# Performance work log

Hardware: AMD Instinct MI355X
Metric: run time of the kernel (lower is better)

The kernel has to match this reference:

```python
import jax, jax.numpy as jnp
import numpy as np

B = 4096
P_HID = 1024
H_HID = 512
MAX_P = 128
MAX_HE = MAX_P // 3  # 42
TAU = 1.0
EPS = 1e-20


def setup_inputs() -> dict:
    key = jax.random.key(0)
    ks = jax.random.split(key, 12)
    s_p = 1.0 / np.sqrt(P_HID)
    s_h = 1.0 / np.sqrt(H_HID)
    # gumbel noise: g = -log(-log(U))
    u_p = jax.random.uniform(ks[3], (B, MAX_P, 2), minval=EPS, maxval=1.0)
    u_h = jax.random.uniform(ks[4], (B, MAX_HE, 2), minval=EPS, maxval=1.0)
    return {
        "particle_h": jax.random.normal(ks[0], (B, P_HID), jnp.float32),
        "edge_h": jax.random.normal(ks[1], (B, H_HID), jnp.float32),
        "hyperedge_h": jax.random.normal(ks[2], (B, H_HID), jnp.float32),
        "g_p": -jnp.log(-jnp.log(u_p)),
        "g_h": -jnp.log(-jnp.log(u_h)),
        "W1_p": jax.random.normal(ks[5], (P_HID, P_HID), jnp.float32) * s_p,
        "b1_p": jnp.zeros((P_HID,), jnp.float32),
        "W2_p": jax.random.normal(ks[6], (P_HID, MAX_P), jnp.float32) * s_p,
        "b2_p": jnp.zeros((MAX_P,), jnp.float32),
        "W1_h": jax.random.normal(ks[7], (H_HID, H_HID), jnp.float32) * s_h,
        "b1_h": jnp.zeros((H_HID,), jnp.float32),
        "W2_h": jax.random.normal(ks[8], (H_HID, MAX_HE), jnp.float32) * s_h,
        "b2_h": jnp.zeros((MAX_HE,), jnp.float32),
    }


def _gumbel_hard_st(logits, g, tau):
    """F.gumbel_softmax(stack([l,-l],-1), tau, hard=True)[...,0] (straight-through)."""
    y = jax.nn.softmax((jnp.stack([logits, -logits], axis=-1) + g) / tau, axis=-1)
    y0 = y[..., 0]
    hard0 = (y0 > y[..., 1]).astype(y0.dtype)
    return hard0 + y0 - jax.lax.stop_gradient(y0)


def _mlp(x, W1, b1, W2, b2):
    return jax.nn.gelu(x @ W1 + b1, approximate=False) @ W2 + b2


def reference(particle_h, edge_h, hyperedge_h, g_p, g_h,
              W1_p, b1_p, W2_p, b2_p, W1_h, b1_h, W2_h, b2_h):
    particle_logits = _mlp(particle_h, W1_p, b1_p, W2_p, b2_p)      # [B, MAX_P]
    particle_mask = _gumbel_hard_st(particle_logits, g_p, TAU)      # [B, MAX_P]
    n_particles = particle_mask.sum(axis=-1).astype(jnp.int32)      # [B]

    # Ragged edge lists as a fixed padded buffer: all C(MAX_P,2) lexicographic
    # pairs (same order as torch.combinations); pair (i,j), i<j, is valid for
    # batch b iff j < n_particles[b].
    ii, jj = jnp.triu_indices(MAX_P, k=1)
    edge_index = jnp.stack([ii, jj]).astype(jnp.int32)              # [2, E_max]
    edge_valid = jj[None, :] < n_particles[:, None]                 # [B, E_max] bool

    hyperedge_logits = _mlp(hyperedge_h, W1_h, b1_h, W2_h, b2_h)    # [B, MAX_HE]
    hyperedge_mask = _gumbel_hard_st(hyperedge_logits, g_h, TAU)
    n_hyperedges = hyperedge_mask.sum(axis=-1).astype(jnp.int32)

    return (particle_mask, n_particles, edge_index, edge_valid,
            hyperedge_mask, n_hyperedges)
```

## Files before the change

kernel.cpp:

```cpp
#include <hip/hip_runtime.h>
#include <hip/hip_bf16.h>
#include <math.h>

typedef __bf16 bf16_t;
typedef bf16_t bf16x8 __attribute__((ext_vector_type(8)));
typedef bf16_t bf16x4 __attribute__((ext_vector_type(4)));
typedef float f32x4 __attribute__((ext_vector_type(4)));
typedef int i32x4 __attribute__((ext_vector_type(4)));
typedef unsigned int u32;

#define B_SZ 4096
#define P_HID 1024
#define H_HID 512
#define MAX_P 128
#define MAX_HE 42
#define HE_PAD 128
#define E_MAX 8128
#define E_MAX4 2032

__device__ __forceinline__ void async_cp16(const bf16_t* g, bf16_t* l) {
    __builtin_amdgcn_global_load_lds(
        (const __attribute__((address_space(1))) u32*)g,
        (__attribute__((address_space(3))) u32*)l, 16, 0, 0);
}

__device__ __forceinline__ float gelu_exact(float v) {
    return 0.5f * v * (1.f + erff(v * 0.70710678118654752f));
}

struct GemmP {
    const bf16_t *Ahi, *Alo, *BThi, *BTlo;
    const float* bias;
    bf16_t *Chi, *Clo;
    const float* g;
    float *out_mask, *out_n;
    int *ws_n;
    int N, K, NV, nx;
};

template<int MODE, int BM>
__global__ __launch_bounds__(256, 3) void gemm_pack(GemmP P, GemmP H, int pBlocks)
{
    constexpr int BN = 128;
    constexpr int MT = BM / 16;
    constexpr int NT = 4;
    constexpr int OPS_A = BM / 16;
    constexpr int OPS_B = BN / 16;
    constexpr int NOPS = 2 * OPS_A + 2 * OPS_B;
    constexpr int TILE = NOPS * 16 * 32;

    __shared__ __align__(16) bf16_t smem[2 * TILE];
    __shared__ float cnt[BM][2];

    const bool isP = (int)blockIdx.x < pBlocks;
    const GemmP& a = isP ? P : H;
    const int bid  = isP ? blockIdx.x : blockIdx.x - pBlocks;
    const int bn   = (bid % a.nx) * BN;
    const int bm   = (bid / a.nx) * BM;
    const int K    = a.K;

    const int tid  = threadIdx.x;
    const int lane = tid & 63;
    const int wid  = tid >> 6;
    const int wn   = wid & 1;
    const int pair = wid >> 1;

    const int srow = lane >> 2;
    const int scol = (lane & 3) * 8;
    const int fr   = lane & 15;
    const int fq   = lane >> 4;

    f32x4 acc[MT][NT];
#pragma unroll
    for (int i = 0; i < MT; ++i)
#pragma unroll
        for (int j = 0; j < NT; ++j)
            acc[i][j] = (f32x4){0.f, 0.f, 0.f, 0.f};

    const bf16_t* const gA0 = a.Ahi  + (size_t)bm * K;
    const bf16_t* const gA1 = a.Alo  + (size_t)bm * K;
    const bf16_t* const gB0 = a.BThi + (size_t)bn * K;
    const bf16_t* const gB1 = a.BTlo + (size_t)bn * K;

    bf16_t* const Tme = smem + pair * TILE;

    for (int kt = 0; kt < K; kt += 64) {
        __syncthreads();
#pragma unroll
        for (int o = 0; o < 2 * NOPS; ++o) {
            if ((o & 3) != wid) continue;
            const int half = (o < NOPS) ? 0 : 1;
            const int oo   = o - half * NOPS;
            const bf16_t* gsrc;
            int q, sec;
            if (oo < OPS_A)                  { q = oo;                     gsrc = gA0; sec = 0; }
            else if (oo < 2 * OPS_A)         { q = oo - OPS_A;             gsrc = gA1; sec = BM * 32; }
            else if (oo < 2 * OPS_A + OPS_B) { q = oo - 2 * OPS_A;         gsrc = gB0; sec = 2 * BM * 32; }
            else                             { q = oo - 2 * OPS_A - OPS_B; gsrc = gB1; sec = 2 * BM * 32 + BN * 32; }
            async_cp16(gsrc + (size_t)(q * 16 + srow) * K + kt + half * 32 + scol,
                       smem + half * TILE + sec + q * 16 * 32);
        }
        __syncthreads();

        bf16x8 ah[MT], al[MT];
#pragma unroll
        for (int i = 0; i < MT; ++i) {
            const int row = i * 16 + fr;
            ah[i] = *(const bf16x8*)(Tme + row * 32 + fq * 8);
            al[i] = *(const bf16x8*)(Tme + BM * 32 + row * 32 + fq * 8);
        }
#pragma unroll
        for (int j = 0; j < NT; ++j) {
            const int row = wn * 64 + j * 16 + fr;
            const bf16x8 bh = *(const bf16x8*)(Tme + 2 * BM * 32 + row * 32 + fq * 8);
            const bf16x8 bl = *(const bf16x8*)(Tme + 2 * BM * 32 + BN * 32 + row * 32 + fq * 8);
#pragma unroll
            for (int i = 0; i < MT; ++i) {
                acc[i][j] = __builtin_amdgcn_mfma_f32_16x16x32_bf16(ah[i], bh, acc[i][j], 0, 0, 0);
                acc[i][j] = __builtin_amdgcn_mfma_f32_16x16x32_bf16(ah[i], bl, acc[i][j], 0, 0, 0);
                acc[i][j] = __builtin_amdgcn_mfma_f32_16x16x32_bf16(al[i], bh, acc[i][j], 0, 0, 0);
            }
        }
    }

    float* const cb = (float*)smem;
    __syncthreads();
    if (pair == 1) {
#pragma unroll
        for (int i = 0; i < MT; ++i)
#pragma unroll
            for (int j = 0; j < NT; ++j)
#pragma unroll
                for (int r = 0; r < 4; ++r)
                    cb[(i * 16 + fq * 4 + r) * BN + wn * 64 + j * 16 + fr] = acc[i][j][r];
    }
    __syncthreads();

    if (pair == 0) {
#pragma unroll
        for (int i = 0; i < MT; ++i)
#pragma unroll
            for (int j = 0; j < NT; ++j)
#pragma unroll
                for (int r = 0; r < 4; ++r)
                    acc[i][j][r] += cb[(i * 16 + fq * 4 + r) * BN + wn * 64 + j * 16 + fr];

        if (MODE == 0) {
#pragma unroll
            for (int i = 0; i < MT; ++i)
#pragma unroll
                for (int j = 0; j < NT; ++j) {
                    const int col  = bn + wn * 64 + j * 16 + fr;
                    const int row0 = bm + i * 16 + fq * 4;
                    const float bj = a.bias[col];
#pragma unroll
                    for (int r = 0; r < 4; ++r) {
                        float v = gelu_exact(acc[i][j][r] + bj);
                        bf16_t h = (bf16_t)v;
                        bf16_t l = (bf16_t)(v - (float)h);
                        const size_t off = (size_t)(row0 + r) * a.N + col;
                        a.Chi[off] = h;
                        a.Clo[off] = l;
                    }
                }
        } else {
            const int NV = a.NV;
#pragma unroll
            for (int i = 0; i < MT; ++i) {
#pragma unroll
                for (int r = 0; r < 4; ++r) {
                    const int row_l = i * 16 + fq * 4 + r;
                    const int grow  = bm + row_l;
                    float s = 0.f;
#pragma unroll
                    for (int j = 0; j < NT; ++j) {
                        const int col = wn * 64 + j * 16 + fr;
                        if (col < NV) {
                            const float v = acc[i][j][r] + a.bias[col];
                            const size_t idx = (size_t)grow * NV + col;
                            const float g0 = a.g[2 * idx + 0];
                            const float g1 = a.g[2 * idx + 1];
                            const float m = ((v + g0) > (g1 - v)) ? 1.f : 0.f;
                            a.out_mask[idx] = m;
                            s += m;
                        }
                    }
                    s += __shfl_xor(s, 1, 64);
                    s += __shfl_xor(s, 2, 64);
                    s += __shfl_xor(s, 4, 64);
                    s += __shfl_xor(s, 8, 64);
                    if (fr == 0) cnt[row_l][wn] = s;
                }
            }
        }
    }

    if (MODE == 1) {
        __syncthreads();
        if (tid < BM) {
            const float c = cnt[tid][0] + cnt[tid][1];
            a.out_n[bm + tid] = c;
            if (a.ws_n) a.ws_n[bm + tid] = (int)c;
        }
    }
}

struct PrepArgs {
    const float *ph, *hh, *W1p, *W2p, *W1h, *W2h;
    bf16_t *pA_hi, *pA_lo, *hA_hi, *hA_lo;
    bf16_t *W1pT_hi, *W1pT_lo, *W2pT_hi, *W2pT_lo;
    bf16_t *W1hT_hi, *W1hT_lo, *W2hT_hi, *W2hT_lo;
    float *out_ei; int *ws_jj;
};

__device__ __forceinline__ void split4(const float* x, bf16_t* hi, bf16_t* lo, int i) {
    float4 v = ((const float4*)x)[i];
    float vv[4] = {v.x, v.y, v.z, v.w};
    bf16x4 h, l;
#pragma unroll
    for (int r = 0; r < 4; ++r) {
        bf16_t hh = (bf16_t)vv[r];
        h[r] = hh;
        l[r] = (bf16_t)(vv[r] - (float)hh);
    }
    ((bf16x4*)hi)[i] = h;
    ((bf16x4*)lo)[i] = l;
}

__device__ __forceinline__ void tsplit(
    const float* W, bf16_t* Thi, bf16_t* Tlo, int K, int N,
    int t, int nx, float (*sh)[33], int tid)
{
    const int n0 = (t % nx) * 32, k0 = (t / nx) * 32;
    const int tx = tid & 31, ty = tid >> 5;
    for (int r = ty; r < 32; r += 8) {
        const int n = n0 + tx;
        sh[r][tx] = (n < N) ? W[(size_t)(k0 + r) * N + n] : 0.f;
    }
    __syncthreads();
    for (int r = ty; r < 32; r += 8) {
        const float x = sh[tx][r];
        bf16_t h = (bf16_t)x;
        bf16_t l = (bf16_t)(x - (float)h);
        const size_t off = (size_t)(n0 + r) * K + k0 + tx;
        Thi[off] = h;
        Tlo[off] = l;
    }
}

__device__ __forceinline__ int tri_off(int i) { return (i * (255 - i)) >> 1; }

__global__ __launch_bounds__(256) void prep_all(PrepArgs a)
{
    __shared__ float sh[32][33];
    const int bid = blockIdx.x;
    const int tid = threadIdx.x;

    if (bid < 4096) {
        split4(a.ph, a.pA_hi, a.pA_lo, bid * 256 + tid);
    } else if (bid < 6144) {
        split4(a.hh, a.hA_hi, a.hA_lo, (bid - 4096) * 256 + tid);
    } else if (bid < 7168) {
        tsplit(a.W1p, a.W1pT_hi, a.W1pT_lo, P_HID, P_HID, bid - 6144, 32, sh, tid);
    } else if (bid < 7296) {
        tsplit(a.W2p, a.W2pT_hi, a.W2pT_lo, P_HID, MAX_P, bid - 7168, 4, sh, tid);
    } else if (bid < 7552) {
        tsplit(a.W1h, a.W1hT_hi, a.W1hT_lo, H_HID, H_HID, bid - 7296, 16, sh, tid);
    } else if (bid < 7616) {
        tsplit(a.W2h, a.W2hT_hi, a.W2hT_lo, H_HID, MAX_HE, bid - 7552, 4, sh, tid);
    } else {
        const int e = (bid - 7616) * 256 + tid;
        if (e < E_MAX) {
            int i = (int)((255.0 - sqrt(65025.0 - 8.0 * (double)e)) * 0.5);
            if (i < 0) i = 0;
            if (i > 126) i = 126;
            while (i > 0 && tri_off(i) > e) --i;
            while (i < 126 && tri_off(i + 1) <= e) ++i;
            const int j = i + 1 + (e - tri_off(i));
            a.out_ei[e] = (float)i;
            a.out_ei[E_MAX + e] = (float)j;
            a.ws_jj[e] = j;
        }
    }
}

__global__ __launch_bounds__(256) void edge_valid_kernel(
    const int* __restrict__ ws_jj, const int* __restrict__ ws_n,
    float* __restrict__ out)
{
    const int b   = blockIdx.x >> 1;
    const int seg = blockIdx.x & 1;
    const int n   = ws_n[b];
    const int base = seg * (E_MAX4 / 2);
    float* const orow = out + (size_t)b * E_MAX;
#pragma unroll
    for (int it = 0; it < 4; ++it) {
        const int q = base + it * 256 + threadIdx.x;
        if (q < base + E_MAX4 / 2) {
            const i32x4 j4 = ((const i32x4*)ws_jj)[q];
            f32x4 v;
            v.x = (j4.x < n) ? 1.f : 0.f;
            v.y = (j4.y < n) ? 1.f : 0.f;
            v.z = (j4.z < n) ? 1.f : 0.f;
            v.w = (j4.w < n) ? 1.f : 0.f;
            __builtin_nontemporal_store(v, &((f32x4*)orow)[q]);
        }
    }
}

extern "C" void kernel_launch(void* const* d_in, const int* in_sizes, int n_in,
                              void* d_out, int out_size, void* d_ws, size_t ws_size,
                              hipStream_t stream)
{
    const float* particle_h  = (const float*)d_in[0];
    const float* hyperedge_h = (const float*)d_in[2];
    const float* g_p  = (const float*)d_in[3];
    const float* g_h  = (const float*)d_in[4];
    const float* W1_p = (const float*)d_in[5];
    const float* b1_p = (const float*)d_in[6];
    const float* W2_p = (const float*)d_in[7];
    const float* b2_p = (const float*)d_in[8];
    const float* W1_h = (const float*)d_in[9];
    const float* b1_h = (const float*)d_in[10];
    const float* W2_h = (const float*)d_in[11];
    const float* b2_h = (const float*)d_in[12];

    float* out = (float*)d_out;
    float* out_pmask = out;
    float* out_np    = out_pmask + (size_t)B_SZ * MAX_P;
    float* out_ei    = out_np + B_SZ;
    float* out_ev    = out_ei + 2 * E_MAX;
    float* out_hmask = out_ev + (size_t)B_SZ * E_MAX;
    float* out_nh    = out_hmask + (size_t)B_SZ * MAX_HE;

    char* w = (char*)d_ws;
    bf16_t* pA_hi   = (bf16_t*)w;  w += (size_t)B_SZ * P_HID * 2;
    bf16_t* pA_lo   = (bf16_t*)w;  w += (size_t)B_SZ * P_HID * 2;
    bf16_t* hA_hi   = (bf16_t*)w;  w += (size_t)B_SZ * H_HID * 2;
    bf16_t* hA_lo   = (bf16_t*)w;  w += (size_t)B_SZ * H_HID * 2;
    bf16_t* hidp_hi = (bf16_t*)w;  w += (size_t)B_SZ * P_HID * 2;
    bf16_t* hidp_lo = (bf16_t*)w;  w += (size_t)B_SZ * P_HID * 2;
    bf16_t* hidh_hi = (bf16_t*)w;  w += (size_t)B_SZ * H_HID * 2;
    bf16_t* hidh_lo = (bf16_t*)w;  w += (size_t)B_SZ * H_HID * 2;
    bf16_t* W1pT_hi = (bf16_t*)w;  w += (size_t)P_HID * P_HID * 2;
    bf16_t* W1pT_lo = (bf16_t*)w;  w += (size_t)P_HID * P_HID * 2;
    bf16_t* W2pT_hi = (bf16_t*)w;  w += (size_t)MAX_P * P_HID * 2;
    bf16_t* W2pT_lo = (bf16_t*)w;  w += (size_t)MAX_P * P_HID * 2;
    bf16_t* W1hT_hi = (bf16_t*)w;  w += (size_t)H_HID * H_HID * 2;
    bf16_t* W1hT_lo = (bf16_t*)w;  w += (size_t)H_HID * H_HID * 2;
    bf16_t* W2hT_hi = (bf16_t*)w;  w += (size_t)HE_PAD * H_HID * 2;
    bf16_t* W2hT_lo = (bf16_t*)w;  w += (size_t)HE_PAD * H_HID * 2;
    int*    ws_np   = (int*)w;     w += B_SZ * 4;
    int*    ws_jj   = (int*)w;

    PrepArgs pa;
    pa.ph = particle_h; pa.hh = hyperedge_h;
    pa.W1p = W1_p; pa.W2p = W2_p; pa.W1h = W1_h; pa.W2h = W2_h;
    pa.pA_hi = pA_hi; pa.pA_lo = pA_lo; pa.hA_hi = hA_hi; pa.hA_lo = hA_lo;
    pa.W1pT_hi = W1pT_hi; pa.W1pT_lo = W1pT_lo;
    pa.W2pT_hi = W2pT_hi; pa.W2pT_lo = W2pT_lo;
    pa.W1hT_hi = W1hT_hi; pa.W1hT_lo = W1hT_lo;
    pa.W2hT_hi = W2hT_hi; pa.W2hT_lo = W2hT_lo;
    pa.out_ei = out_ei; pa.ws_jj = ws_jj;
    prep_all<<<7648, 256, 0, stream>>>(pa);

    {
        GemmP P = {}, H = {};
        P.Ahi = pA_hi;  P.Alo = pA_lo;  P.BThi = W1pT_hi; P.BTlo = W1pT_lo;
        P.bias = b1_p;  P.Chi = hidp_hi; P.Clo = hidp_lo;
        P.N = P_HID; P.K = P_HID; P.nx = P_HID / 128;
        H.Ahi = hA_hi;  H.Alo = hA_lo;  H.BThi = W1hT_hi; H.BTlo = W1hT_lo;
        H.bias = b1_h;  H.Chi = hidh_hi; H.Clo = hidh_lo;
        H.N = H_HID; H.K = H_HID; H.nx = H_HID / 128;
        const int pB = (B_SZ / 64) * P.nx;
        const int hB = (B_SZ / 64) * H.nx;
        gemm_pack<0, 64><<<pB + hB, 256, 0, stream>>>(P, H, pB);
    }

    {
        GemmP P = {}, H = {};
        P.Ahi = hidp_hi; P.Alo = hidp_lo; P.BThi = W2pT_hi; P.BTlo = W2pT_lo;
        P.bias = b2_p; P.g = g_p; P.out_mask = out_pmask; P.out_n = out_np;
        P.ws_n = ws_np; P.N = MAX_P; P.K = P_HID; P.NV = MAX_P; P.nx = 1;
        H.Ahi = hidh_hi; H.Alo = hidh_lo; H.BThi = W2hT_hi; H.BTlo = W2hT_lo;
        H.bias = b2_h; H.g = g_h; H.out_mask = out_hmask; H.out_n = out_nh;
        H.ws_n = nullptr; H.N = HE_PAD; H.K = H_HID; H.NV = MAX_HE; H.nx = 1;
        const int pB = B_SZ / 32;
        const int hB = B_SZ / 32;
        gemm_pack<1, 32><<<pB + hB, 256, 0, stream>>>(P, H, pB);
    }

    edge_valid_kernel<<<2 * B_SZ, 256, 0, stream>>>(ws_jj, ws_np, out_ev);
}
```

Before: 287.1 us.

## Double-buffer K tiles and split warps over M instead of split-K pairs

Replaces the split-K scheme, where two warp pairs each handled half of a 64-wide K step and were reduced through shared memory, with a 2x2 warp tiling over M and N on 32-wide K steps. The two shared-memory buffers now form a double buffer: the next tile is staged asynchronously while the current one feeds the MFMAs. This removes one barrier per iteration and the final cross-pair reduction through LDS, and is meant to overlap global-to-LDS copies with matrix math. In exchange the K loop has twice as many iterations, each with less work. Correctness depends on global_load_lds finishing before the single barrier at the end of each iteration.

```diff
diff --git a/kernel.cpp b/kernel.cpp
--- a/kernel.cpp
+++ b/kernel.cpp
@@ -42,7 +42,7 @@
 __global__ __launch_bounds__(256, 3) void gemm_pack(GemmP P, GemmP H, int pBlocks)
 {
     constexpr int BN = 128;
-    constexpr int MT = BM / 16;
+    constexpr int MT = BM / 32;
     constexpr int NT = 4;
     constexpr int OPS_A = BM / 16;
     constexpr int OPS_B = BN / 16;
@@ -62,8 +62,8 @@
     const int tid  = threadIdx.x;
     const int lane = tid & 63;
     const int wid  = tid >> 6;
-    const int wn   = wid & 1;
-    const int pair = wid >> 1;
+    const int wm   = wid & 1;
+    const int wn   = wid >> 1;
 
     const int srow = lane >> 2;
     const int scol = (lane & 3) * 8;
@@ -82,38 +82,40 @@
     const bf16_t* const gB0 = a.BThi + (size_t)bn * K;
     const bf16_t* const gB1 = a.BTlo + (size_t)bn * K;
 
-    bf16_t* const Tme = smem + pair * TILE;
-
-    for (int kt = 0; kt < K; kt += 64) {
-        __syncthreads();
-#pragma unroll
-        for (int o = 0; o < 2 * NOPS; ++o) {
+    auto stage = [&](int buf, int kt) {
+#pragma unroll
+        for (int o = 0; o < NOPS; ++o) {
             if ((o & 3) != wid) continue;
-            const int half = (o < NOPS) ? 0 : 1;
-            const int oo   = o - half * NOPS;
             const bf16_t* gsrc;
             int q, sec;
-            if (oo < OPS_A)                  { q = oo;                     gsrc = gA0; sec = 0; }
-            else if (oo < 2 * OPS_A)         { q = oo - OPS_A;             gsrc = gA1; sec = BM * 32; }
-            else if (oo < 2 * OPS_A + OPS_B) { q = oo - 2 * OPS_A;         gsrc = gB0; sec = 2 * BM * 32; }
-            else                             { q = oo - 2 * OPS_A - OPS_B; gsrc = gB1; sec = 2 * BM * 32 + BN * 32; }
-            async_cp16(gsrc + (size_t)(q * 16 + srow) * K + kt + half * 32 + scol,
-                       smem + half * TILE + sec + q * 16 * 32);
-        }
-        __syncthreads();
-
+            if (o < OPS_A)                  { q = o;                     gsrc = gA0; sec = 0; }
+            else if (o < 2 * OPS_A)         { q = o - OPS_A;             gsrc = gA1; sec = BM * 32; }
+            else if (o < 2 * OPS_A + OPS_B) { q = o - 2 * OPS_A;         gsrc = gB0; sec = 2 * BM * 32; }
+            else                            { q = o - 2 * OPS_A - OPS_B; gsrc = gB1; sec = 2 * BM * 32 + BN * 32; }
+            async_cp16(gsrc + (size_t)(q * 16 + srow) * K + kt + scol,
+                       smem + buf * TILE + sec + q * 16 * 32);
+        }
+    };
+
+    stage(0, 0);
+    __syncthreads();
+    int cur = 0;
+    for (int kt = 0; kt < K; kt += 32) {
+        if (kt + 32 < K) stage(cur ^ 1, kt + 32);
+
+        const bf16_t* const Tb = smem + cur * TILE;
         bf16x8 ah[MT], al[MT];
 #pragma unroll
         for (int i = 0; i < MT; ++i) {
-            const int row = i * 16 + fr;
-            ah[i] = *(const bf16x8*)(Tme + row * 32 + fq * 8);
-            al[i] = *(const bf16x8*)(Tme + BM * 32 + row * 32 + fq * 8);
+            const int row = wm * (BM / 2) + i * 16 + fr;
+            ah[i] = *(const bf16x8*)(Tb + row * 32 + fq * 8);
+            al[i] = *(const bf16x8*)(Tb + BM * 32 + row * 32 + fq * 8);
         }
 #pragma unroll
         for (int j = 0; j < NT; ++j) {
             const int row = wn * 64 + j * 16 + fr;
-            const bf16x8 bh = *(const bf16x8*)(Tme + 2 * BM * 32 + row * 32 + fq * 8);
-            const bf16x8 bl = *(const bf16x8*)(Tme + 2 * BM * 32 + BN * 32 + row * 32 + fq * 8);
+            const bf16x8 bh = *(const bf16x8*)(Tb + 2 * BM * 32 + row * 32 + fq * 8);
+            const bf16x8 bl = *(const bf16x8*)(Tb + 2 * BM * 32 + BN * 32 + row * 32 + fq * 8);
 #pragma unroll
             for (int i = 0; i < MT; ++i) {
                 acc[i][j] = __builtin_amdgcn_mfma_f32_16x16x32_bf16(ah[i], bh, acc[i][j], 0, 0, 0);
@@ -121,81 +123,57 @@
                 acc[i][j] = __builtin_amdgcn_mfma_f32_16x16x32_bf16(al[i], bh, acc[i][j], 0, 0, 0);
             }
         }
-    }
-
-    float* const cb = (float*)smem;
-    __syncthreads();
-    if (pair == 1) {
+        __syncthreads();
+        cur ^= 1;
+    }
+
+    if (MODE == 0) {
 #pragma unroll
         for (int i = 0; i < MT; ++i)
 #pragma unroll
-            for (int j = 0; j < NT; ++j)
-#pragma unroll
-                for (int r = 0; r < 4; ++r)
-                    cb[(i * 16 + fq * 4 + r) * BN + wn * 64 + j * 16 + fr] = acc[i][j][r];
-    }
-    __syncthreads();
-
-    if (pair == 0) {
-#pragma unroll
-        for (int i = 0; i < MT; ++i)
-#pragma unroll
-            for (int j = 0; j < NT; ++j)
-#pragma unroll
-                for (int r = 0; r < 4; ++r)
-                    acc[i][j][r] += cb[(i * 16 + fq * 4 + r) * BN + wn * 64 + j * 16 + fr];
-
-        if (MODE == 0) {
-#pragma unroll
-            for (int i = 0; i < MT; ++i)
+            for (int j = 0; j < NT; ++j) {
+                const int col  = bn + wn * 64 + j * 16 + fr;
+                const int row0 = bm + wm * (BM / 2) + i * 16 + fq * 4;
+                const float bj = a.bias[col];
+#pragma unroll
+                for (int r = 0; r < 4; ++r) {
+                    float v = gelu_exact(acc[i][j][r] + bj);
+                    bf16_t h = (bf16_t)v;
+                    bf16_t l = (bf16_t)(v - (float)h);
+                    const size_t off = (size_t)(row0 + r) * a.N + col;
+                    a.Chi[off] = h;
+                    a.Clo[off] = l;
+                }
+            }
+    } else {
+        const int NV = a.NV;
+#pragma unroll
+        for (int i = 0; i < MT; ++i) {
+#pragma unroll
+            for (int r = 0; r < 4; ++r) {
+                const int row_l = wm * (BM / 2) + i * 16 + fq * 4 + r;
+                const int grow  = bm + row_l;
+                float s = 0.f;
 #pragma unroll
                 for (int j = 0; j < NT; ++j) {
-                    const int col  = bn + wn * 64 + j * 16 + fr;
-                    const int row0 = bm + i * 16 + fq * 4;
-                    const float bj = a.bias[col];
-#pragma unroll
-                    for (int r = 0; r < 4; ++r) {
-                        float v = gelu_exact(acc[i][j][r] + bj);
-                        bf16_t h = (bf16_t)v;
-                        bf16_t l = (bf16_t)(v - (float)h);
-                        const size_t off = (size_t)(row0 + r) * a.N + col;
-                        a.Chi[off] = h;
-                        a.Clo[off] = l;
+                    const int col = wn * 64 + j * 16 + fr;
+                    if (col < NV) {
+                        const float v = acc[i][j][r] + a.bias[col];
+                        const size_t idx = (size_t)grow * NV + col;
+                        const float g0 = a.g[2 * idx + 0];
+                        const float g1 = a.g[2 * idx + 1];
+                        const float m = ((v + g0) > (g1 - v)) ? 1.f : 0.f;
+                        a.out_mask[idx] = m;
+                        s += m;
                     }
                 }
-        } else {
-            const int NV = a.NV;
-#pragma unroll
-            for (int i = 0; i < MT; ++i) {
-#pragma unroll
-                for (int r = 0; r < 4; ++r) {
-                    const int row_l = i * 16 + fq * 4 + r;
-                    const int grow  = bm + row_l;
-                    float s = 0.f;
-#pragma unroll
-                    for (int j = 0; j < NT; ++j) {
-                        const int col = wn * 64 + j * 16 + fr;
-                        if (col < NV) {
-                            const float v = acc[i][j][r] + a.bias[col];
-                            const size_t idx = (size_t)grow * NV + col;
-                            const float g0 = a.g[2 * idx + 0];
-                            const float g1 = a.g[2 * idx + 1];
-                            const float m = ((v + g0) > (g1 - v)) ? 1.f : 0.f;
-                            a.out_mask[idx] = m;
-                            s += m;
-                        }
-                    }
-                    s += __shfl_xor(s, 1, 64);
-                    s += __shfl_xor(s, 2, 64);
-                    s += __shfl_xor(s, 4, 64);
-                    s += __shfl_xor(s, 8, 64);
-                    if (fr == 0) cnt[row_l][wn] = s;
-                }
+                s += __shfl_xor(s, 1, 64);
+                s += __shfl_xor(s, 2, 64);
+                s += __shfl_xor(s, 4, 64);
+                s += __shfl_xor(s, 8, 64);
+                if (fr == 0) cnt[row_l][wn] = s;
             }
         }
-    }
-
-    if (MODE == 1) {
         __syncthreads();
         if (tid < BM) {
             const float c = cnt[tid][0] + cnt[tid][1];
```

Measured after the change: 274.4 us. 1.05x faster.
